# Performance work log

Hardware: AMD Instinct MI355X
Metric: run time of the kernel (lower is better)

## Reference

```python
import jax, jax.numpy as jnp
import numpy as np

N_TOKEN = 256
C_PAIR = 128
C = 32
N_HEADS = 4
LN_EPS = 1e-5


def setup_inputs() -> dict:
    key = jax.random.key(0)
    ks = jax.random.split(key, 8)
    w = lambda k, shape: jax.random.normal(k, shape, dtype=jnp.float32) * 0.02
    return {
        "pair": jax.random.normal(ks[0], (N_TOKEN, N_TOKEN, C_PAIR), dtype=jnp.float32),
        "gamma": jnp.ones((C_PAIR,), dtype=jnp.float32),
        "beta": jnp.zeros((C_PAIR,), dtype=jnp.float32),
        "Wq": w(ks[1], (C_PAIR, C * N_HEADS)),
        "Wk": w(ks[2], (C_PAIR, C * N_HEADS)),
        "Wv": w(ks[3], (C_PAIR, C * N_HEADS)),
        "Wb": w(ks[4], (C_PAIR, N_HEADS)),
        "Wg": w(ks[5], (C_PAIR, C * N_HEADS)),
        "Wout": w(ks[6], (C * N_HEADS, C_PAIR)),
    }


def _layernorm(x, gamma, beta):
    mu = jnp.mean(x, axis=-1, keepdims=True)
    var = jnp.mean(jnp.square(x - mu), axis=-1, keepdims=True)
    return (x - mu) * jax.lax.rsqrt(var + LN_EPS) * gamma + beta


def reference(pair, gamma, beta, Wq, Wk, Wv, Wb, Wg, Wout):
    n = pair.shape[0]
    pn = _layernorm(pair, gamma, beta)  # [N, N, c_pair]
    q = (pn @ Wq).reshape(n, n, N_HEADS, C)  # [i, j, h, c]
    k = (pn @ Wk).reshape(n, n, N_HEADS, C)  # [i, k, h, c]
    v = (pn @ Wv).reshape(n, n, N_HEADS, C)
    b = pn @ Wb                               # [j, k, h] pairwise bias
    g = jax.nn.sigmoid(pn @ Wg).reshape(n, n, N_HEADS, C)
    # a^h_ijk = softmax_k( q_ij . k_ik / sqrt(c) + b_jk )
    logits = jnp.einsum("ijhc,ikhc->ijkh", q, k) / np.float32(np.sqrt(C))
    logits = logits + b[None, :, :, :]        # broadcast over i: bias indexed by (j, k)
    attn = jax.nn.softmax(logits, axis=2)     # softmax over k axis
    o = jnp.einsum("ijkh,ikhc->ijhc", attn, v) * g
    return o.reshape(n, n, N_HEADS * C) @ Wout  # [N, N, c_pair]
```

## Files before the change

kernel.cpp:

```cpp
#include <hip/hip_runtime.h>

#define N_TOK 256
#define CP    128
#define CHD   32
#define NH    4
#define NT    65536
#define NCOL  528
#define VTP   268
#define SP    134

typedef short short8 __attribute__((ext_vector_type(8)));
typedef float f32x4  __attribute__((ext_vector_type(4)));
typedef float f32x2  __attribute__((ext_vector_type(2)));

__device__ __forceinline__ short f2bf(float f) {
    unsigned u = __builtin_bit_cast(unsigned, f);
    u += 0x7fffu + ((u >> 16) & 1u);
    return (short)(u >> 16);
}
__device__ __forceinline__ float bf2f(short s) {
    unsigned u = ((unsigned)(unsigned short)s) << 16;
    return __builtin_bit_cast(float, u);
}

__global__ void pack_weights(const float* __restrict__ Wq, const float* __restrict__ Wk,
                             const float* __restrict__ Wv, const float* __restrict__ Wb,
                             const float* __restrict__ Wg, const float* __restrict__ Wout,
                             short* __restrict__ wcat, short* __restrict__ woutT) {
    int idx = blockIdx.x * 256 + threadIdx.x;
    if (idx < NCOL * CP) {
        int n = idx >> 7, k = idx & 127;
        float v = 0.f;
        if (n < 512) {
            const float* W = (n < 128) ? Wq : (n < 256) ? Wk : (n < 384) ? Wv : Wg;
            int col = (n & 96) + 2 * (n & 15) + ((n >> 4) & 1);
            v = W[k * 128 + col];
            if (n < 128) v *= 0.17677669529663687f;
        } else if (n < 516) {
            v = Wb[k * 4 + (n - 512)];
        }
        wcat[n * CP + k] = f2bf(v);
    } else {
        int j = idx - NCOL * CP;
        if (j < 128 * 128) {
            int n = j >> 7, k = j & 127;
            int col = (n & 96) + 2 * (n & 15) + ((n >> 4) & 1);
            woutT[n * 128 + k] = f2bf(Wout[k * 128 + col]);
        }
    }
}

__global__ __launch_bounds__(256, 4)
void ln_proj(const float* __restrict__ pair, const float* __restrict__ gamma,
             const float* __restrict__ beta, const short* __restrict__ wcat,
             short* __restrict__ qt, short* __restrict__ kt,
             short* __restrict__ vt, short* __restrict__ gt,
             float* __restrict__ bt) {
    __shared__ short pn[10240];
    const int tid = threadIdx.x;
    const int wv = tid >> 6, lane = tid & 63;
    const int quad = lane >> 4, l15 = lane & 15;
    const int r0 = blockIdx.x * 64;
    short* const ST = &pn[wv * 2560];

    float ga0 = gamma[2 * lane], ga1 = gamma[2 * lane + 1];
    float be0 = beta[2 * lane],  be1 = beta[2 * lane + 1];

    #pragma unroll 4
    for (int rr = 0; rr < 16; ++rr) {
        int row = wv * 16 + rr;
        const float* src = pair + (size_t)(r0 + row) * CP + 2 * lane;
        float x0 = src[0], x1 = src[1];
        float s = x0 + x1;
        #pragma unroll
        for (int m = 32; m; m >>= 1) s += __shfl_xor(s, m);
        float mu = s * (1.f / 128.f);
        float d0 = x0 - mu, d1 = x1 - mu;
        float vs = d0 * d0 + d1 * d1;
        #pragma unroll
        for (int m = 32; m; m >>= 1) vs += __shfl_xor(vs, m);
        float rs = rsqrtf(vs * (1.f / 128.f) + 1e-5f);
        short y0 = f2bf(d0 * rs * ga0 + be0);
        short y1 = f2bf(d1 * rs * ga1 + be1);
        unsigned pk = ((unsigned)(unsigned short)y0) | (((unsigned)(unsigned short)y1) << 16);
        *(unsigned*)&pn[row * 136 + 2 * lane] = pk;
    }
    __syncthreads();

    short8 af[4][4];
    #pragma unroll
    for (int rt = 0; rt < 4; ++rt)
        #pragma unroll
        for (int s = 0; s < 4; ++s)
            af[rt][s] = *(const short8*)&pn[(rt * 16 + l15) * 136 + s * 32 + quad * 8];
    __syncthreads();

    short* const dst = (wv == 0) ? qt : (wv == 1) ? kt : (wv == 2) ? vt : gt;

#define LOADB(BUF, CHN) {                                                          \
        int n_ = (CHN) * 16 + l15;                                                 \
        _Pragma("unroll")                                                          \
        for (int s = 0; s < 4; ++s)                                                \
            BUF[s] = *(const short8*)&wcat[(size_t)n_ * CP + s * 32 + quad * 8];   \
    }

#define EVEN(BUF) {                                                                \
        _Pragma("unroll")                                                          \
        for (int rt = 0; rt < 4; ++rt) {                                           \
            f32x4 a = {0.f, 0.f, 0.f, 0.f};                                        \
            _Pragma("unroll")                                                      \
            for (int s = 0; s < 4; ++s)                                            \
                a = __builtin_amdgcn_mfma_f32_16x16x32_bf16(af[rt][s], BUF[s], a, 0, 0, 0); \
            accE[rt] = a;                                                          \
        }                                                                          \
    }

#define ODD(CC, BUF) {                                                             \
        const int chn = wv * 8 + (CC);                                             \
        const int h_ = (chn >> 1) & 3;                                             \
        _Pragma("unroll")                                                          \
        for (int rt = 0; rt < 4; ++rt) {                                           \
            f32x4 a = {0.f, 0.f, 0.f, 0.f};                                        \
            _Pragma("unroll")                                                      \
            for (int s = 0; s < 4; ++s)                                            \
                a = __builtin_amdgcn_mfma_f32_16x16x32_bf16(af[rt][s], BUF[s], a, 0, 0, 0); \
            _Pragma("unroll")                                                      \
            for (int r = 0; r < 4; ++r) {                                          \
                int rowl = rt * 16 + quad * 4 + r;                                 \
                float ve = accE[rt][r], vo = a[r];                                 \
                if (wv == 3) {                                                     \
                    ve = 1.f / (1.f + __expf(-ve));                                \
                    vo = 1.f / (1.f + __expf(-vo));                                \
                }                                                                  \
                unsigned pk = ((unsigned)(unsigned short)f2bf(ve))                 \
                            | (((unsigned)(unsigned short)f2bf(vo)) << 16);        \
                *(unsigned*)&ST[rowl * 40 + 2 * l15] = pk;                         \
            }                                                                      \
        }                                                                          \
        const size_t hb2 = (size_t)h_ * NT * CHD + (size_t)r0 * CHD;               \
        _Pragma("unroll")                                                          \
        for (int s = 0; s < 4; ++s) {                                              \
            int f = s * 64 + lane;                                                 \
            int row = f >> 2, cs = (f & 3) * 8;                                    \
            short8 v = *(const short8*)&ST[row * 40 + cs];                         \
            *(short8*)(dst + hb2 + (size_t)row * CHD + cs) = v;                    \
        }                                                                          \
    }

    short8 bA[4], bB[4];
    f32x4 accE[4];
    LOADB(bA, wv * 8 + 0)
    LOADB(bB, wv * 8 + 1)
    EVEN(bA) LOADB(bA, wv * 8 + 2)
    ODD(1, bB) LOADB(bB, wv * 8 + 3)
    EVEN(bA) LOADB(bA, wv * 8 + 4)
    ODD(3, bB) LOADB(bB, wv * 8 + 5)
    EVEN(bA) LOADB(bA, wv * 8 + 6)
    ODD(5, bB) LOADB(bB, wv * 8 + 7)
    EVEN(bA) LOADB(bA, wv * 8 + 8)
    ODD(7, bB)

    if (wv == 3) {
        #pragma unroll
        for (int rt = 0; rt < 4; ++rt) {
            f32x4 acc = {0.f, 0.f, 0.f, 0.f};
            #pragma unroll
            for (int s = 0; s < 4; ++s)
                acc = __builtin_amdgcn_mfma_f32_16x16x32_bf16(af[rt][s], bA[s], acc, 0, 0, 0);
            if (l15 < 4) {
                #pragma unroll
                for (int r = 0; r < 4; ++r) {
                    int gr = r0 + rt * 16 + quad * 4 + r;
                    bt[l15 * NT + gr] = acc[r];
                }
            }
        }
    }
#undef LOADB
#undef EVEN
#undef ODD
}

__global__ __launch_bounds__(256)
void bias_T(const float* __restrict__ bt, float* __restrict__ btT) {
    __shared__ float t[64][65];
    int bid = blockIdx.x;
    int h = bid >> 4, tj = (bid >> 2) & 3, tk = bid & 3;
    const float* src = bt + (size_t)h * NT;
    float* dstp = btT + (size_t)h * NT;
    int c = threadIdx.x & 63, r4 = threadIdx.x >> 6;
    #pragma unroll
    for (int rr = 0; rr < 16; ++rr) {
        int r = rr * 4 + r4;
        t[r][c] = src[(size_t)(tj * 64 + r) * 256 + tk * 64 + c];
    }
    __syncthreads();
    #pragma unroll
    for (int rr = 0; rr < 16; ++rr) {
        int k = rr * 4 + r4;
        dstp[(size_t)(tk * 64 + k) * 256 + tj * 64 + c] = t[c][k];
    }
}

__global__ __launch_bounds__(256)
void attn(const short* __restrict__ qt, const short* __restrict__ kt,
          const short* __restrict__ vt, const short* __restrict__ gt,
          const float* __restrict__ btT, short* __restrict__ og) {
    __shared__ short vT[32 * VTP];
    __shared__ short pl[4 * 16 * SP];
    const int tid = threadIdx.x;
    const int h = blockIdx.x >> 8, i = blockIdx.x & 255;
    const int wv = tid >> 6, lane = tid & 63;
    const int quad = lane >> 4, l15 = lane & 15;
    short* const strip = &pl[wv * 16 * SP];

    const short* kbase = kt + ((size_t)h * NT + (size_t)i * 256) * CHD;
    const short* vbase = vt + ((size_t)h * NT + (size_t)i * 256) * CHD;
    const short* qbase = qt + ((size_t)h * NT + (size_t)i * 256) * CHD;
    const short* gbase = gt + ((size_t)h * NT + (size_t)i * 256) * CHD;
    const float* btTb = btT + (size_t)h * NT;

    for (int g = tid; g < 1024; g += 256) {
        int key = g >> 2, p = g & 3;
        short8 s = *(const short8*)(vbase + key * CHD + p * 8);
        #pragma unroll
        for (int cc = 0; cc < 8; ++cc) {
            int c = p * 8 + cc;
            int row = (c & 1) ? 16 + (c >> 1) : (c >> 1);
            vT[row * VTP + key] = s[cc];
        }
    }
    __syncthreads();

    for (int jt = 0; jt < 4; ++jt) {
        int jbase = jt * 64 + wv * 16;
        short8 aq = *(const short8*)(qbase + (jbase + l15) * CHD + quad * 8);

        f32x4 sacc[16];
        __builtin_amdgcn_s_setprio(1);
        #pragma unroll
        for (int t = 0; t < 16; ++t) {
            f32x4 c = *(const f32x4*)(btTb + (size_t)(t * 16 + l15) * 256 + jbase + quad * 4);
            short8 bk = *(const short8*)(kbase + (t * 16 + l15) * CHD + quad * 8);
            sacc[t] = __builtin_amdgcn_mfma_f32_16x16x32_bf16(aq, bk, c, 0, 0, 0);
        }
        __builtin_amdgcn_s_setprio(0);
        float sm[4] = {0.f, 0.f, 0.f, 0.f};
        #pragma unroll
        for (int t = 0; t < 16; ++t)
            #pragma unroll
            for (int r = 0; r < 4; ++r) {
                float e = __expf(sacc[t][r]);
                sacc[t][r] = e;
                sm[r] += e;
            }
        #pragma unroll
        for (int m = 1; m < 16; m <<= 1)
            #pragma unroll
            for (int r = 0; r < 4; ++r) sm[r] += __shfl_xor(sm[r], m, 16);
        float inv[4];
        #pragma unroll
        for (int r = 0; r < 4; ++r) inv[r] = 1.f / sm[r];

        f32x4 oacc[2];
        oacc[0] = f32x4{0.f, 0.f, 0.f, 0.f};
        oacc[1] = f32x4{0.f, 0.f, 0.f, 0.f};
        #pragma unroll
        for (int t = 0; t < 8; ++t)
            #pragma unroll
            for (int r = 0; r < 4; ++r)
                strip[(quad * 4 + r) * SP + t * 16 + l15] = f2bf(sacc[t][r]);
        __builtin_amdgcn_s_setprio(1);
        #pragma unroll
        for (int ks = 0; ks < 4; ++ks) {
            short8 ap = *(const short8*)&strip[l15 * SP + ks * 32 + quad * 8];
            #pragma unroll
            for (int nt = 0; nt < 2; ++nt) {
                short8 bv = *(const short8*)&vT[(nt * 16 + l15) * VTP + ks * 32 + quad * 8];
                oacc[nt] = __builtin_amdgcn_mfma_f32_16x16x32_bf16(ap, bv, oacc[nt], 0, 0, 0);
            }
        }
        __builtin_amdgcn_s_setprio(0);
        #pragma unroll
        for (int t = 8; t < 16; ++t)
            #pragma unroll
            for (int r = 0; r < 4; ++r)
                strip[(quad * 4 + r) * SP + (t - 8) * 16 + l15] = f2bf(sacc[t][r]);
        __builtin_amdgcn_s_setprio(1);
        #pragma unroll
        for (int ks = 4; ks < 8; ++ks) {
            short8 ap = *(const short8*)&strip[l15 * SP + (ks - 4) * 32 + quad * 8];
            #pragma unroll
            for (int nt = 0; nt < 2; ++nt) {
                short8 bv = *(const short8*)&vT[(nt * 16 + l15) * VTP + ks * 32 + quad * 8];
                oacc[nt] = __builtin_amdgcn_mfma_f32_16x16x32_bf16(ap, bv, oacc[nt], 0, 0, 0);
            }
        }
        __builtin_amdgcn_s_setprio(0);
        #pragma unroll
        for (int r = 0; r < 4; ++r) {
            int j = jbase + quad * 4 + r;
            unsigned gw = *(const unsigned*)(gbase + (size_t)j * CHD + 2 * l15);
            float g0 = bf2f((short)(gw & 0xffff)) * inv[r];
            float g1 = bf2f((short)(gw >> 16)) * inv[r];
            unsigned pk = ((unsigned)(unsigned short)f2bf(oacc[0][r] * g0))
                        | (((unsigned)(unsigned short)f2bf(oacc[1][r] * g1)) << 16);
            *(unsigned*)&og[((size_t)i * 256 + j) * CP + h * CHD + 2 * l15] = pk;
        }
    }
}

__global__ __launch_bounds__(256)
void out_gemm(const short* __restrict__ og, const short* __restrict__ woutT,
              float* __restrict__ out) {
    __shared__ short al[64 * 136];
    const int tid = threadIdx.x;
    const int wv = tid >> 6, lane = tid & 63;
    const int quad = lane >> 4, l15 = lane & 15;
    const int r0 = blockIdx.x * 64;

    for (int g = tid; g < 1024; g += 256) {
        int row = g >> 4, p = g & 15;
        *(short8*)&al[row * 136 + p * 8] = *(const short8*)(og + (size_t)(r0 + row) * CP + p * 8);
    }
    __syncthreads();

    short8 af[4][4];
    #pragma unroll
    for (int rt = 0; rt < 4; ++rt)
        #pragma unroll
        for (int s = 0; s < 4; ++s)
            af[rt][s] = *(const short8*)&al[(rt * 16 + l15) * 136 + s * 32 + quad * 8];

    short8 bE[4], bO[4];
    #pragma unroll
    for (int s = 0; s < 4; ++s) {
        bE[s] = *(const short8*)&woutT[(size_t)(wv * 32 + l15) * 128 + s * 32 + quad * 8];
        bO[s] = *(const short8*)&woutT[(size_t)(wv * 32 + 16 + l15) * 128 + s * 32 + quad * 8];
    }

    #pragma unroll
    for (int rt = 0; rt < 4; ++rt) {
        f32x4 accE = {0.f, 0.f, 0.f, 0.f}, accO = {0.f, 0.f, 0.f, 0.f};
        #pragma unroll
        for (int s = 0; s < 4; ++s) {
            accE = __builtin_amdgcn_mfma_f32_16x16x32_bf16(af[rt][s], bE[s], accE, 0, 0, 0);
            accO = __builtin_amdgcn_mfma_f32_16x16x32_bf16(af[rt][s], bO[s], accO, 0, 0, 0);
        }
        #pragma unroll
        for (int r = 0; r < 4; ++r) {
            f32x2 pk = {accE[r], accO[r]};
            *(f32x2*)&out[(size_t)(r0 + rt * 16 + quad * 4 + r) * CP + wv * 32 + 2 * l15] = pk;
        }
    }
}

extern "C" void kernel_launch(void* const* d_in, const int* in_sizes, int n_in,
                              void* d_out, int out_size, void* d_ws, size_t ws_size,
                              hipStream_t stream) {
    (void)in_sizes; (void)n_in; (void)out_size; (void)ws_size;
    const float* pair  = (const float*)d_in[0];
    const float* gamma = (const float*)d_in[1];
    const float* beta  = (const float*)d_in[2];
    const float* Wq    = (const float*)d_in[3];
    const float* Wk    = (const float*)d_in[4];
    const float* Wv    = (const float*)d_in[5];
    const float* Wb    = (const float*)d_in[6];
    const float* Wg    = (const float*)d_in[7];
    const float* Wout  = (const float*)d_in[8];
    float* out = (float*)d_out;

    char* ws = (char*)d_ws;
    const size_t SZ_QKVG = (size_t)NH * NT * CHD * 2;
    short* wcat  = (short*)(ws);
    short* woutT = (short*)(ws + 135168);
    short* qt    = (short*)(ws + 167936);
    short* kt    = (short*)(ws + 167936 + SZ_QKVG);
    short* vt    = (short*)(ws + 167936 + 2 * SZ_QKVG);
    short* gt    = (short*)(ws + 167936 + 3 * SZ_QKVG);
    float* bt    = (float*)(ws + 167936 + 4 * SZ_QKVG);
    float* btT   = (float*)(ws + 167936 + 4 * SZ_QKVG + (size_t)NH * NT * 4);
    short* og    = (short*)(ws + 167936 + 4 * SZ_QKVG + 2 * (size_t)NH * NT * 4);

    hipLaunchKernelGGL(pack_weights, dim3(328), dim3(256), 0, stream,
                       Wq, Wk, Wv, Wb, Wg, Wout, wcat, woutT);
    hipLaunchKernelGGL(ln_proj, dim3(1024), dim3(256), 0, stream,
                       pair, gamma, beta, wcat, qt, kt, vt, gt, bt);
    hipLaunchKernelGGL(bias_T, dim3(64), dim3(256), 0, stream, bt, btT);
    hipLaunchKernelGGL(attn, dim3(1024), dim3(256), 0, stream,
                       qt, kt, vt, gt, btT, og);
    hipLaunchKernelGGL(out_gemm, dim3(1024), dim3(256), 0, stream,
                       og, woutT, out);
}
```

Before: 202.4 us.

## Split logits into two halves, stage full P strip in LDS, raise occupancy

```diff
diff --git a/kernel.cpp b/kernel.cpp
--- a/kernel.cpp
+++ b/kernel.cpp
@@ -7,7 +7,6 @@
 #define NT    65536
 #define NCOL  528
 #define VTP   268
-#define SP    134
 
 typedef short short8 __attribute__((ext_vector_type(8)));
 typedef float f32x4  __attribute__((ext_vector_type(4)));
@@ -202,17 +201,16 @@
     }
 }
 
-__global__ __launch_bounds__(256)
+__global__ __launch_bounds__(256, 3)
 void attn(const short* __restrict__ qt, const short* __restrict__ kt,
           const short* __restrict__ vt, const short* __restrict__ gt,
           const float* __restrict__ btT, short* __restrict__ og) {
     __shared__ short vT[32 * VTP];
-    __shared__ short pl[4 * 16 * SP];
+    __shared__ short pl[64 * VTP];
     const int tid = threadIdx.x;
     const int h = blockIdx.x >> 8, i = blockIdx.x & 255;
     const int wv = tid >> 6, lane = tid & 63;
     const int quad = lane >> 4, l15 = lane & 15;
-    short* const strip = &pl[wv * 16 * SP];
 
     const short* kbase = kt + ((size_t)h * NT + (size_t)i * 256) * CHD;
     const short* vbase = vt + ((size_t)h * NT + (size_t)i * 256) * CHD;
@@ -235,25 +233,38 @@
     for (int jt = 0; jt < 4; ++jt) {
         int jbase = jt * 64 + wv * 16;
         short8 aq = *(const short8*)(qbase + (jbase + l15) * CHD + quad * 8);
-
-        f32x4 sacc[16];
-        __builtin_amdgcn_s_setprio(1);
-        #pragma unroll
-        for (int t = 0; t < 16; ++t) {
-            f32x4 c = *(const f32x4*)(btTb + (size_t)(t * 16 + l15) * 256 + jbase + quad * 4);
-            short8 bk = *(const short8*)(kbase + (t * 16 + l15) * CHD + quad * 8);
-            sacc[t] = __builtin_amdgcn_mfma_f32_16x16x32_bf16(aq, bk, c, 0, 0, 0);
-        }
-        __builtin_amdgcn_s_setprio(0);
+        unsigned gw = *(const unsigned*)(gbase + (size_t)(jbase + quad * 4) * CHD + 2 * l15);
+        unsigned gw1 = *(const unsigned*)(gbase + (size_t)(jbase + quad * 4 + 1) * CHD + 2 * l15);
+        unsigned gw2 = *(const unsigned*)(gbase + (size_t)(jbase + quad * 4 + 2) * CHD + 2 * l15);
+        unsigned gw3 = *(const unsigned*)(gbase + (size_t)(jbase + quad * 4 + 3) * CHD + 2 * l15);
+
         float sm[4] = {0.f, 0.f, 0.f, 0.f};
         #pragma unroll
-        for (int t = 0; t < 16; ++t)
-            #pragma unroll
-            for (int r = 0; r < 4; ++r) {
-                float e = __expf(sacc[t][r]);
-                sacc[t][r] = e;
-                sm[r] += e;
+        for (int kh = 0; kh < 2; ++kh) {
+            f32x4 sacc[8];
+            __builtin_amdgcn_s_setprio(1);
+            #pragma unroll
+            for (int t = 0; t < 8; ++t) {
+                int tt = kh * 8 + t;
+                f32x4 c = *(const f32x4*)(btTb + (size_t)(tt * 16 + l15) * 256 + jbase + quad * 4);
+                short8 bk = *(const short8*)(kbase + (tt * 16 + l15) * CHD + quad * 8);
+                sacc[t] = __builtin_amdgcn_mfma_f32_16x16x32_bf16(aq, bk, c, 0, 0, 0);
             }
+            __builtin_amdgcn_s_setprio(0);
+            #pragma unroll
+            for (int t = 0; t < 8; ++t)
+                #pragma unroll
+                for (int r = 0; r < 4; ++r) {
+                    float e = __expf(sacc[t][r]);
+                    sacc[t][r] = e;
+                    sm[r] += e;
+                }
+            #pragma unroll
+            for (int t = 0; t < 8; ++t)
+                #pragma unroll
+                for (int r = 0; r < 4; ++r)
+                    pl[(wv * 16 + quad * 4 + r) * VTP + (kh * 8 + t) * 16 + l15] = f2bf(sacc[t][r]);
+        }
         #pragma unroll
         for (int m = 1; m < 16; m <<= 1)
             #pragma unroll
@@ -265,15 +276,10 @@
         f32x4 oacc[2];
         oacc[0] = f32x4{0.f, 0.f, 0.f, 0.f};
         oacc[1] = f32x4{0.f, 0.f, 0.f, 0.f};
-        #pragma unroll
-        for (int t = 0; t < 8; ++t)
-            #pragma unroll
-            for (int r = 0; r < 4; ++r)
-                strip[(quad * 4 + r) * SP + t * 16 + l15] = f2bf(sacc[t][r]);
         __builtin_amdgcn_s_setprio(1);
         #pragma unroll
-        for (int ks = 0; ks < 4; ++ks) {
-            short8 ap = *(const short8*)&strip[l15 * SP + ks * 32 + quad * 8];
+        for (int ks = 0; ks < 8; ++ks) {
+            short8 ap = *(const short8*)&pl[(wv * 16 + l15) * VTP + ks * 32 + quad * 8];
             #pragma unroll
             for (int nt = 0; nt < 2; ++nt) {
                 short8 bv = *(const short8*)&vT[(nt * 16 + l15) * VTP + ks * 32 + quad * 8];
@@ -281,28 +287,12 @@
             }
         }
         __builtin_amdgcn_s_setprio(0);
-        #pragma unroll
-        for (int t = 8; t < 16; ++t)
-            #pragma unroll
-            for (int r = 0; r < 4; ++r)
-                strip[(quad * 4 + r) * SP + (t - 8) * 16 + l15] = f2bf(sacc[t][r]);
-        __builtin_amdgcn_s_setprio(1);
-        #pragma unroll
-        for (int ks = 4; ks < 8; ++ks) {
-            short8 ap = *(const short8*)&strip[l15 * SP + (ks - 4) * 32 + quad * 8];
-            #pragma unroll
-            for (int nt = 0; nt < 2; ++nt) {
-                short8 bv = *(const short8*)&vT[(nt * 16 + l15) * VTP + ks * 32 + quad * 8];
-                oacc[nt] = __builtin_amdgcn_mfma_f32_16x16x32_bf16(ap, bv, oacc[nt], 0, 0, 0);
-            }
-        }
-        __builtin_amdgcn_s_setprio(0);
+        unsigned gws[4] = {gw, gw1, gw2, gw3};
         #pragma unroll
         for (int r = 0; r < 4; ++r) {
             int j = jbase + quad * 4 + r;
-            unsigned gw = *(const unsigned*)(gbase + (size_t)j * CHD + 2 * l15);
-            float g0 = bf2f((short)(gw & 0xffff)) * inv[r];
-            float g1 = bf2f((short)(gw >> 16)) * inv[r];
+            float g0 = bf2f((short)(gws[r] & 0xffff)) * inv[r];
+            float g1 = bf2f((short)(gws[r] >> 16)) * inv[r];
             unsigned pk = ((unsigned)(unsigned short)f2bf(oacc[0][r] * g0))
                         | (((unsigned)(unsigned short)f2bf(oacc[1][r] * g1)) << 16);
             *(unsigned*)&og[((size_t)i * 256 + j) * CP + h * CHD + 2 * l15] = pk;
```

Result: faster. 189.6 us (-6.3%).
